# Kernel tuning notes

Hardware: AMD Instinct MI355X
Metric: run time of the kernel (lower is better)

## Reference

```python
import jax, jax.numpy as jnp
import numpy as np

BN_EPS = 1e-5


def setup_inputs() -> dict:
    key = jax.random.key(0)
    ks = jax.random.split(key, 7)
    B, C, N = 8, 512, 2048
    P = C // 2
    x = jax.random.normal(ks[0], (B, C, N), dtype=jnp.float32)
    # 1x1 conv weights (no bias), shape [out, in]
    Wg = jax.random.normal(ks[1], (P, C), dtype=jnp.float32) * (1.0 / np.sqrt(C))
    Wtheta = jax.random.normal(ks[2], (P, C), dtype=jnp.float32) * (1.0 / np.sqrt(C))
    Wphi = jax.random.normal(ks[3], (P, C), dtype=jnp.float32) * (1.0 / np.sqrt(C))
    Wz = jax.random.normal(ks[4], (C, P), dtype=jnp.float32) * (1.0 / np.sqrt(P))
    gamma = jnp.ones((C,), dtype=jnp.float32)
    beta = jnp.zeros((C,), dtype=jnp.float32)
    return {"x": x, "Wg": Wg, "Wtheta": Wtheta, "Wphi": Wphi, "Wz": Wz,
            "gamma": gamma, "beta": beta}


def reference(x, Wg, Wtheta, Wphi, Wz, gamma, beta):
    # x: [B, C, N]
    g = jnp.einsum('pc,bcn->bnp', Wg, x)        # [B, N, P]
    theta = jnp.einsum('pc,bcn->bnp', Wtheta, x)  # [B, N, P]
    phi = jnp.einsum('pc,bcn->bpn', Wphi, x)      # [B, P, N]
    f = jnp.einsum('bnp,bpm->bnm', theta, phi)    # [B, N, N] unscaled scores
    f = jax.nn.softmax(f, axis=-1)
    y = jnp.einsum('bnm,bmp->bpn', f, g)          # [B, P, N]
    z = jnp.einsum('cp,bpn->bcn', Wz, y)          # [B, C, N]
    # BatchNorm1d (training-mode batch stats over batch and length dims)
    mean = jnp.mean(z, axis=(0, 2), keepdims=True)
    var = jnp.mean((z - mean) ** 2, axis=(0, 2), keepdims=True)
    z_bn = (z - mean) / jnp.sqrt(var + BN_EPS)
    z_bn = z_bn * gamma[None, :, None] + beta[None, :, None]
    return z_bn + x
```

## Files before the change

kernel.cpp:

```cpp
#include <hip/hip_runtime.h>
#include <hip/hip_bf16.h>


typedef __attribute__((ext_vector_type(8))) short short8;
typedef __attribute__((ext_vector_type(4))) float floatx4;

__device__ __forceinline__ unsigned short f2bf(float v) {
    __hip_bfloat16 h = __float2bfloat16(v);
    return *(unsigned short*)&h;
}
__device__ __forceinline__ float bf2f(unsigned short u) {
    __hip_bfloat16 h;
    *(unsigned short*)&h = u;
    return __bfloat162float(h);
}

__device__ __forceinline__ void gl16(const unsigned short* g, unsigned short* l) {
    __builtin_amdgcn_global_load_lds(
        (const __attribute__((address_space(1))) unsigned int*)g,
        (__attribute__((address_space(3))) unsigned int*)l, 16, 0, 0);
}

__global__ __launch_bounds__(256) void transpose_split(
    const float* __restrict__ X, unsigned short* __restrict__ Thi,
    unsigned short* __restrict__ Tlo, int R, int N)
{
    X   += (long)blockIdx.z * R * N;
    Thi += (long)blockIdx.z * N * R;
    Tlo += (long)blockIdx.z * N * R;
    __shared__ float s[32][133];
    const int t = threadIdx.x;
    const int n0 = blockIdx.x * 128, r0 = blockIdx.y * 32;
    const int nf = (t & 31) * 4, rf = t >> 5;
#pragma unroll
    for (int rr = 0; rr < 4; ++rr) {
        const int row = rf + rr * 8;
        const float4 v = *(const float4*)&X[(long)(r0 + row) * N + n0 + nf];
        s[row][nf]     = v.x;
        s[row][nf + 1] = v.y;
        s[row][nf + 2] = v.z;
        s[row][nf + 3] = v.w;
    }
    __syncthreads();
    const int n = t >> 1, rs = (t & 1) * 16;
    short8 h0, h1, l0, l1;
#pragma unroll
    for (int j = 0; j < 8; ++j) {
        const float v = s[rs + j][n];
        const unsigned short h = f2bf(v);
        h0[j] = (short)h;
        l0[j] = (short)f2bf(v - bf2f(h));
    }
#pragma unroll
    for (int j = 0; j < 8; ++j) {
        const float v = s[rs + 8 + j][n];
        const unsigned short h = f2bf(v);
        h1[j] = (short)h;
        l1[j] = (short)f2bf(v - bf2f(h));
    }
    const long ob = (long)(n0 + n) * R + r0 + rs;
    *(short8*)&Thi[ob]     = h0;
    *(short8*)&Thi[ob + 8] = h1;
    *(short8*)&Tlo[ob]     = l0;
    *(short8*)&Tlo[ob + 8] = l1;
}

__global__ __launch_bounds__(256) void split_w2(
    const float* __restrict__ Wth, const float* __restrict__ Wph,
    unsigned short* __restrict__ Whi, unsigned short* __restrict__ Wlo, int PC)
{
    const int i = blockIdx.x * 256 + threadIdx.x;
    if (i < 2 * PC) {
        const float v = (i < PC) ? Wth[i] : Wph[i - PC];
        const unsigned short hi = f2bf(v);
        Whi[i] = hi;
        Wlo[i] = f2bf(v - bf2f(hi));
    }
}

__global__ __launch_bounds__(256) void cast_bf16(
    const float* __restrict__ X, unsigned short* __restrict__ Y)
{
    const long i = ((long)blockIdx.x * 256 + threadIdx.x) * 4;
    const float4 v = *(const float4*)&X[i];
    ushort4 o;
    o.x = f2bf(v.x); o.y = f2bf(v.y); o.z = f2bf(v.z); o.w = f2bf(v.w);
    *(ushort4*)&Y[i] = o;
}

#define BK 32

template <bool SPLIT, int OUTMODE, int FM, int FN, bool XYSWAP>
__global__ __launch_bounds__(256) void mfma_gemm(
    const unsigned short* __restrict__ Ahi, const unsigned short* __restrict__ Alo,
    const unsigned short* __restrict__ Bhi, const unsigned short* __restrict__ Blo,
    void* __restrict__ Cout, void* __restrict__ Cout2,
    int K, int lda, int ldb, int ldc,
    long sA, long sB, long sC,
    float* __restrict__ S1, float* __restrict__ S2)
{
    constexpr int MTM = FM * 32, MTN = FN * 32;
    constexpr int SA = FM / 2, SB = FN / 2;
    constexpr int ASZ = MTM * BK, BSZ = MTN * BK;

    Ahi += (long)blockIdx.z * sA;
    Bhi += (long)blockIdx.z * sB;
    if (SPLIT) { Alo += (long)blockIdx.z * sA; Blo += (long)blockIdx.z * sB; }
    float* Cf = (float*)Cout + (long)blockIdx.z * sC;
    unsigned short* Ch = (unsigned short*)Cout + (long)blockIdx.z * sC;
    unsigned short* Cl = (unsigned short*)Cout2 + (long)blockIdx.z * sC;

    __shared__ unsigned short AsH[2 * ASZ], BsH[2 * BSZ];
    __shared__ unsigned short AsL[SPLIT ? 2 * ASZ : 8], BsL[SPLIT ? 2 * BSZ : 8];

    const int tid = threadIdx.x;
    const int wid = tid >> 6, lane = tid & 63;
    const int wm = (wid >> 1) * (FM * 16), wn = (wid & 1) * (FN * 16);
    const int l15 = lane & 15, quad = lane >> 4;
    const int m0 = (XYSWAP ? blockIdx.x : blockIdx.y) * MTM;
    const int n0 = (XYSWAP ? blockIdx.y : blockIdx.x) * MTN;

    int arow[SA], acol[SA], brow[SB], bcol[SB];
#pragma unroll
    for (int t = 0; t < SA; ++t) {
        const int gid = t * 256 + tid;
        arow[t] = gid >> 2; acol[t] = (gid & 3) * 8;
    }
#pragma unroll
    for (int t = 0; t < SB; ++t) {
        const int gid = t * 256 + tid;
        brow[t] = gid >> 2; bcol[t] = (gid & 3) * 8;
    }

    auto stage = [&](int k0, int buf) {
#pragma unroll
        for (int t = 0; t < SA; ++t) {
            const long o = (long)(m0 + arow[t]) * lda + k0 + acol[t];
            const int d = buf * ASZ + (t * 256 + tid) * 8;
            gl16(&Ahi[o], &AsH[d]);
            if (SPLIT) gl16(&Alo[o], &AsL[d]);
        }
#pragma unroll
        for (int t = 0; t < SB; ++t) {
            const long o = (long)(n0 + brow[t]) * ldb + k0 + bcol[t];
            const int d = buf * BSZ + (t * 256 + tid) * 8;
            gl16(&Bhi[o], &BsH[d]);
            if (SPLIT) gl16(&Blo[o], &BsL[d]);
        }
    };

    floatx4 acc[FM][FN];
#pragma unroll
    for (int i = 0; i < FM; ++i)
#pragma unroll
        for (int j = 0; j < FN; ++j) acc[i][j] = (floatx4){0.f, 0.f, 0.f, 0.f};

    const int iters = K / BK;
    stage(0, 0);
    __syncthreads();

    for (int it = 0; it < iters; ++it) {
        const int cur = it & 1;
        if (it + 1 < iters) stage((it + 1) * BK, cur ^ 1);

        short8 ah[FM], bh[FN], al[SPLIT ? FM : 1], bl[SPLIT ? FN : 1];
#pragma unroll
        for (int i = 0; i < FM; ++i) {
            ah[i] = *(const short8*)&AsH[cur * ASZ + (wm + i * 16 + l15) * BK + quad * 8];
            if (SPLIT) al[i] = *(const short8*)&AsL[cur * ASZ + (wm + i * 16 + l15) * BK + quad * 8];
        }
#pragma unroll
        for (int j = 0; j < FN; ++j) {
            bh[j] = *(const short8*)&BsH[cur * BSZ + (wn + j * 16 + l15) * BK + quad * 8];
            if (SPLIT) bl[j] = *(const short8*)&BsL[cur * BSZ + (wn + j * 16 + l15) * BK + quad * 8];
        }
#pragma unroll
        for (int i = 0; i < FM; ++i)
#pragma unroll
            for (int j = 0; j < FN; ++j) {
                acc[i][j] = __builtin_amdgcn_mfma_f32_16x16x32_bf16(ah[i], bh[j], acc[i][j], 0, 0, 0);
                if (SPLIT) {
                    acc[i][j] = __builtin_amdgcn_mfma_f32_16x16x32_bf16(ah[i], bl[j], acc[i][j], 0, 0, 0);
                    acc[i][j] = __builtin_amdgcn_mfma_f32_16x16x32_bf16(al[i], bh[j], acc[i][j], 0, 0, 0);
                }
            }

        __syncthreads();
    }

#pragma unroll
    for (int i = 0; i < FM; ++i)
#pragma unroll
        for (int j = 0; j < FN; ++j) {
            const int m = m0 + wm + i * 16 + quad * 4;
            const int n = n0 + wn + j * 16 + l15;
#pragma unroll
            for (int r = 0; r < 4; ++r) {
                const float v = acc[i][j][r];
                const long idx = (long)(m + r) * ldc + n;
                if (OUTMODE == 0) {
                    Cf[idx] = v;
                } else if (OUTMODE == 1 || OUTMODE == 3) {
                    Ch[idx] = f2bf(v);
                } else {
                    const unsigned short hi = f2bf(v);
                    Ch[idx] = hi;
                    Cl[idx] = f2bf(v - bf2f(hi));
                }
            }
        }

    if (OUTMODE == 3) {
        const int slot = (blockIdx.z * gridDim.x + blockIdx.x) * 2 + (wn >> 6);
#pragma unroll
        for (int i = 0; i < FM; ++i)
#pragma unroll
            for (int r = 0; r < 4; ++r) {
                float s = 0.f, q = 0.f;
#pragma unroll
                for (int j = 0; j < FN; ++j) {
                    const float v = acc[i][j][r];
                    s += v; q += v * v;
                }
#pragma unroll
                for (int msk = 1; msk < 16; msk <<= 1) {
                    s += __shfl_xor(s, msk, 64);
                    q += __shfl_xor(q, msk, 64);
                }
                if (l15 == 0) {
                    const int row = m0 + wm + i * 16 + quad * 4 + r;
                    S1[(long)row * 256 + slot] = s;
                    S2[(long)row * 256 + slot] = q;
                }
            }
    }
}

#define PSTRP 136

__device__ __forceinline__ int swz64(int row, int slot) {
    return (row << 6) + (((slot ^ row) & 7) << 3);
}

__global__ __launch_bounds__(256, 2) void fused_attn(
    const unsigned short* __restrict__ thphH,
    const unsigned short* __restrict__ thphL,
    const unsigned short* __restrict__ gbf,
    float* __restrict__ yp,
    float2* __restrict__ ml)
{
    const int N = 2048, P = 256, P2 = 512;
    const int id = blockIdx.x;
    const int b  = id & 7;
    const int kh = (id >> 3) & 1;
    const int qt = id >> 4;
    const int q0 = qt * 64;

    const unsigned short* thB = thphH + (long)b * N * P2;
    const unsigned short* tlB = thphL + (long)b * N * P2;
    const unsigned short* gB  = gbf   + (long)b * P * N;
    float*  ypB = yp + (long)kh * (8L * N * P) + (long)b * N * P;
    float2* mlB = ml + (long)kh * (8L * N) + (long)b * N;

    __shared__ unsigned short FG[2 * 128 * 64];
    unsigned short* Fh = FG;
    unsigned short* Fl = FG + 128 * 64;
    unsigned short* Gs = FG;
    __shared__ unsigned short Pw[4][16 * PSTRP];
    __shared__ float Aly[64];

    const int tid = threadIdx.x;
    const int wid = tid >> 6, lane = tid & 63;
    const int l15 = lane & 15, quad = lane >> 4;

    short8 tHr[8], tLr[8];
    {
        const unsigned short* t1 = thB + (long)(q0 + wid * 16 + l15) * P2;
        const unsigned short* t2 = tlB + (long)(q0 + wid * 16 + l15) * P2;
#pragma unroll
        for (int kt = 0; kt < 8; ++kt) {
            tHr[kt] = *(const short8*)&t1[kt * 32 + quad * 8];
            tLr[kt] = *(const short8*)&t2[kt * 32 + quad * 8];
        }
    }

    float mrun[4], lrun[4];
#pragma unroll
    for (int r = 0; r < 4; ++r) { mrun[r] = -1e30f; lrun[r] = 0.f; }

    floatx4 oacc[16];
#pragma unroll
    for (int p = 0; p < 16; ++p) oacc[p] = (floatx4){0.f, 0.f, 0.f, 0.f};

    const int prow4 = tid >> 2, lslot = tid & 3;
    short8 pfH[2][2], pfL[2][2];
    short8 pg[2][4];

    for (int mt = 0; mt < 8; ++mt) {
        const int m0 = kh * 1024 + mt * 128;

        floatx4 sacc[8];
#pragma unroll
        for (int j = 0; j < 8; ++j) sacc[j] = (floatx4){0.f, 0.f, 0.f, 0.f};

#pragma unroll
        for (int s = 0; s < 2; ++s) {
            const long o = (long)(m0 + s * 64 + prow4) * P2 + P + 0 * 32 + lslot * 8;
            pfH[0][s] = *(const short8*)&thB[o];
            pfL[0][s] = *(const short8*)&tlB[o];
        }
#pragma unroll
        for (int s = 0; s < 2; ++s) {
            const int row = s * 64 + prow4;
            *(short8*)&Fh[swz64(row, lslot)] = pfH[0][s];
            *(short8*)&Fl[swz64(row, lslot)] = pfL[0][s];
        }
#pragma unroll
        for (int s = 0; s < 2; ++s) {
            const long o = (long)(m0 + s * 64 + prow4) * P2 + P + 1 * 32 + lslot * 8;
            pfH[1][s] = *(const short8*)&thB[o];
            pfL[1][s] = *(const short8*)&tlB[o];
        }
        __syncthreads();

#pragma unroll
        for (int kc = 0; kc < 8; ++kc) {
            if (kc < 6) {
#pragma unroll
                for (int s = 0; s < 2; ++s) {
                    const long o = (long)(m0 + s * 64 + prow4) * P2 + P + (kc + 2) * 32 + lslot * 8;
                    pfH[kc & 1][s] = *(const short8*)&thB[o];
                    pfL[kc & 1][s] = *(const short8*)&tlB[o];
                }
            }
            const short8 aH = tHr[kc];
            const short8 aL = tLr[kc];
            const int half = (kc & 1) * 4;
            __builtin_amdgcn_s_setprio(1);
#pragma unroll
            for (int j = 0; j < 8; ++j) {
                const int ro = swz64(j * 16 + l15, half + quad);
                const short8 bh = *(const short8*)&Fh[ro];
                const short8 bl = *(const short8*)&Fl[ro];
                sacc[j] = __builtin_amdgcn_mfma_f32_16x16x32_bf16(aH, bh, sacc[j], 0, 0, 0);
                sacc[j] = __builtin_amdgcn_mfma_f32_16x16x32_bf16(aH, bl, sacc[j], 0, 0, 0);
                sacc[j] = __builtin_amdgcn_mfma_f32_16x16x32_bf16(aL, bh, sacc[j], 0, 0, 0);
            }
            __builtin_amdgcn_s_setprio(0);
            if (kc < 7) {
                const int wh = ((kc + 1) & 1) * 4;
#pragma unroll
                for (int s = 0; s < 2; ++s) {
                    const int row = s * 64 + prow4;
                    *(short8*)&Fh[swz64(row, wh + lslot)] = pfH[(kc + 1) & 1][s];
                    *(short8*)&Fl[swz64(row, wh + lslot)] = pfL[(kc + 1) & 1][s];
                }
            }
            __syncthreads();
        }

        float alpha[4];
#pragma unroll
        for (int r = 0; r < 4; ++r) {
            float v = sacc[0][r];
#pragma unroll
            for (int j = 1; j < 8; ++j) v = fmaxf(v, sacc[j][r]);
            v = fmaxf(v, __shfl_xor(v, 1, 64));
            v = fmaxf(v, __shfl_xor(v, 2, 64));
            v = fmaxf(v, __shfl_xor(v, 4, 64));
            v = fmaxf(v, __shfl_xor(v, 8, 64));
            const float mo = mrun[r];
            const float mn = fmaxf(mo, v);
            mrun[r] = mn;
            alpha[r] = __expf(mo - mn);
        }
        float lpart[4] = {0.f, 0.f, 0.f, 0.f};
#pragma unroll
        for (int j = 0; j < 8; ++j)
#pragma unroll
            for (int r = 0; r < 4; ++r) {
                const float p = __expf(sacc[j][r] - mrun[r]);
                Pw[wid][(quad * 4 + r) * PSTRP + j * 16 + l15] = f2bf(p);
                lpart[r] += p;
            }
#pragma unroll
        for (int r = 0; r < 4; ++r) {
            float s = lpart[r];
            s += __shfl_xor(s, 1, 64);
            s += __shfl_xor(s, 2, 64);
            s += __shfl_xor(s, 4, 64);
            s += __shfl_xor(s, 8, 64);
            lrun[r] = lrun[r] * alpha[r] + s;
        }
        if (l15 == 0) {
#pragma unroll
            for (int r = 0; r < 4; ++r) Aly[wid * 16 + quad * 4 + r] = alpha[r];
        }

#pragma unroll
        for (int s = 0; s < 4; ++s)
            pg[0][s] = *(const short8*)&gB[(long)(s * 64 + prow4) * N + m0 + 0 * 32 + lslot * 8];
#pragma unroll
        for (int s = 0; s < 4; ++s)
            *(short8*)&Gs[swz64(s * 64 + prow4, lslot)] = pg[0][s];
#pragma unroll
        for (int s = 0; s < 4; ++s)
            pg[1][s] = *(const short8*)&gB[(long)(s * 64 + prow4) * N + m0 + 1 * 32 + lslot * 8];
        __syncthreads();

        float alr[4][4];
#pragma unroll
        for (int g = 0; g < 4; ++g)
#pragma unroll
            for (int r = 0; r < 4; ++r) alr[g][r] = Aly[g * 16 + quad * 4 + r];
        int noresc = 1;
#pragma unroll
        for (int g = 0; g < 4; ++g)
#pragma unroll
            for (int r = 0; r < 4; ++r) noresc &= (alr[g][r] == 1.f);
        if (!__all(noresc)) {
#pragma unroll
            for (int g = 0; g < 4; ++g)
#pragma unroll
                for (int pj = 0; pj < 4; ++pj)
#pragma unroll
                    for (int r = 0; r < 4; ++r) oacc[g * 4 + pj][r] *= alr[g][r];
        }

#pragma unroll
        for (int mc = 0; mc < 4; ++mc) {
            if (mc < 2) {
#pragma unroll
                for (int s = 0; s < 4; ++s)
                    pg[mc & 1][s] = *(const short8*)&gB[(long)(s * 64 + prow4) * N + m0 + (mc + 2) * 32 + lslot * 8];
            }
            const int half = (mc & 1) * 4;
            short8 af[4];
#pragma unroll
            for (int g = 0; g < 4; ++g)
                af[g] = *(const short8*)&Pw[g][l15 * PSTRP + mc * 32 + quad * 8];
            __builtin_amdgcn_s_setprio(1);
#pragma unroll
            for (int pj = 0; pj < 4; ++pj) {
                const short8 bg = *(const short8*)&Gs[swz64(wid * 64 + pj * 16 + l15, half + quad)];
#pragma unroll
                for (int g = 0; g < 4; ++g)
                    oacc[g * 4 + pj] = __builtin_amdgcn_mfma_f32_16x16x32_bf16(af[g], bg, oacc[g * 4 + pj], 0, 0, 0);
            }
            __builtin_amdgcn_s_setprio(0);
            if (mc < 3) {
                const int wh = ((mc + 1) & 1) * 4;
#pragma unroll
                for (int s = 0; s < 4; ++s)
                    *(short8*)&Gs[swz64(s * 64 + prow4, wh + lslot)] = pg[(mc + 1) & 1][s];
                __syncthreads();
            }
        }
    }

    if (l15 == 0) {
#pragma unroll
        for (int r = 0; r < 4; ++r) Aly[wid * 16 + quad * 4 + r] = 1.0f / lrun[r];
    }
    __syncthreads();
    float liv[4][4];
#pragma unroll
    for (int g = 0; g < 4; ++g)
#pragma unroll
        for (int r = 0; r < 4; ++r) liv[g][r] = Aly[g * 16 + quad * 4 + r];
#pragma unroll
    for (int g = 0; g < 4; ++g)
#pragma unroll
        for (int pj = 0; pj < 4; ++pj)
#pragma unroll
            for (int r = 0; r < 4; ++r) {
                const int row = q0 + g * 16 + quad * 4 + r;
                const int col = wid * 64 + pj * 16 + l15;
                ypB[(long)row * P + col] = oacc[g * 4 + pj][r] * liv[g][r];
            }
    if (l15 == 0) {
#pragma unroll
        for (int r = 0; r < 4; ++r) {
            const int row = q0 + wid * 16 + quad * 4 + r;
            mlB[row] = float2{mrun[r], lrun[r]};
        }
    }
}

__global__ __launch_bounds__(256) void attn_merge(
    const float* __restrict__ yp, const float2* __restrict__ ml,
    unsigned short* __restrict__ ybf)
{
    const long HALF = 8L * 2048 * 256;
    const long t = (long)blockIdx.x * 256 + threadIdx.x;
    const long row = t >> 5;
    const int  c0  = ((int)t & 31) * 8;
    const float2 a = ml[row];
    const float2 c = ml[8L * 2048 + row];
    const float mx = fmaxf(a.x, c.x);
    const float w1 = a.y * __expf(a.x - mx);
    const float w2 = c.y * __expf(c.x - mx);
    const float inv = 1.0f / (w1 + w2);
    const float f1 = w1 * inv, f2 = w2 * inv;
    const long base = row * 256 + c0;
    const float4 u0 = *(const float4*)&yp[base];
    const float4 u1 = *(const float4*)&yp[base + 4];
    const float4 v0 = *(const float4*)&yp[HALF + base];
    const float4 v1 = *(const float4*)&yp[HALF + base + 4];
    ushort4 o0, o1;
    o0.x = f2bf(f1 * u0.x + f2 * v0.x);
    o0.y = f2bf(f1 * u0.y + f2 * v0.y);
    o0.z = f2bf(f1 * u0.z + f2 * v0.z);
    o0.w = f2bf(f1 * u0.w + f2 * v0.w);
    o1.x = f2bf(f1 * u1.x + f2 * v1.x);
    o1.y = f2bf(f1 * u1.y + f2 * v1.y);
    o1.z = f2bf(f1 * u1.z + f2 * v1.z);
    o1.w = f2bf(f1 * u1.w + f2 * v1.w);
    *(ushort4*)&ybf[base] = o0;
    *(ushort4*)&ybf[base + 4] = o1;
}

__global__ __launch_bounds__(256) void bn_finalize(
    const float* __restrict__ p1, const float* __restrict__ p2,
    float* __restrict__ mean, float* __restrict__ rstd, float cnt)
{
    const int c = blockIdx.x, t = threadIdx.x;
    __shared__ float rs[256], rq[256];
    rs[t] = p1[(long)c * 256 + t];
    rq[t] = p2[(long)c * 256 + t];
    __syncthreads();
    for (int st = 128; st > 0; st >>= 1) {
        if (t < st) { rs[t] += rs[t + st]; rq[t] += rq[t + st]; }
        __syncthreads();
    }
    if (t == 0) {
        const float m = rs[0] / cnt;
        mean[c] = m;
        rstd[c] = rsqrtf(rq[0] / cnt - m * m + 1e-5f);
    }
}

__global__ __launch_bounds__(256) void bn_apply_bf(
    const unsigned short* __restrict__ z, const float* __restrict__ x,
    const float* __restrict__ mean, const float* __restrict__ rstd,
    const float* __restrict__ gamma, const float* __restrict__ beta,
    float* __restrict__ out)
{
    const long i = ((long)blockIdx.x * 256 + threadIdx.x) * 8;
    const int c = (int)((i >> 11) & 511);
    const float mu = mean[c], rs = rstd[c], ga = gamma[c], be = beta[c];
    const ushort4 z0 = *(const ushort4*)&z[i];
    const ushort4 z1 = *(const ushort4*)&z[i + 4];
    const float4 x0 = *(const float4*)&x[i];
    const float4 x1 = *(const float4*)&x[i + 4];
    float4 o0, o1;
    o0.x = (bf2f(z0.x) - mu) * rs * ga + be + x0.x;
    o0.y = (bf2f(z0.y) - mu) * rs * ga + be + x0.y;
    o0.z = (bf2f(z0.z) - mu) * rs * ga + be + x0.z;
    o0.w = (bf2f(z0.w) - mu) * rs * ga + be + x0.w;
    o1.x = (bf2f(z1.x) - mu) * rs * ga + be + x1.x;
    o1.y = (bf2f(z1.y) - mu) * rs * ga + be + x1.y;
    o1.z = (bf2f(z1.z) - mu) * rs * ga + be + x1.z;
    o1.w = (bf2f(z1.w) - mu) * rs * ga + be + x1.w;
    *(float4*)&out[i] = o0;
    *(float4*)&out[i + 4] = o1;
}

extern "C" void kernel_launch(void* const* d_in, const int* in_sizes, int n_in,
                              void* d_out, int out_size, void* d_ws, size_t ws_size,
                              hipStream_t stream)
{
    const int B = 8, C = 512, N = 2048, P = 256;
    const float* x      = (const float*)d_in[0];
    const float* Wg     = (const float*)d_in[1];
    const float* Wtheta = (const float*)d_in[2];
    const float* Wphi   = (const float*)d_in[3];
    const float* Wz     = (const float*)d_in[4];
    const float* gamma  = (const float*)d_in[5];
    const float* beta   = (const float*)d_in[6];
    float* out = (float*)d_out;

    float* ws = (float*)d_ws;
    const long NCle = (long)N * C;
    const long NP   = (long)N * P;
    const long R0   = (long)B * NCle;
    unsigned short* xtH   = (unsigned short*)ws;
    unsigned short* xtL   = xtH + B * NCle;
    unsigned short* zbf   = (unsigned short*)ws;
    unsigned short* thphH = (unsigned short*)(ws + R0);
    unsigned short* thphL = thphH + B * NCle;
    unsigned short* gbf   = (unsigned short*)(ws + 2 * R0);
    unsigned short* fbf   = gbf + B * NP;
    unsigned short* ybf   = fbf + (long)B * N * N;
    unsigned short* W2H   = ybf + B * NP;
    unsigned short* W2L   = W2H + 2L * P * C;
    unsigned short* WgB   = W2L + 2L * P * C;
    unsigned short* WzB   = WgB + (long)P * C;
    float*          yp    = (float*)fbf;
    float2*         ml    = (float2*)(ws + 6L * 1024 * 1024);
    float*          bnp1  = ws + R0;
    float*          bnp2  = bnp1 + (long)C * 256;
    float*          mean  = bnp2 + (long)C * 256;
    float*          rstd  = mean + C;

    const long sX = (long)C * N;
    const int  P2 = 2 * P;

    transpose_split<<<dim3(N / 128, C / 32, B), 256, 0, stream>>>(x, xtH, xtL, C, N);
    split_w2<<<(2 * P * C + 255) / 256, 256, 0, stream>>>(Wtheta, Wphi, W2H, W2L, P * C);
    cast_bf16<<<P * C / 1024, 256, 0, stream>>>(Wg, WgB);
    cast_bf16<<<P * C / 1024, 256, 0, stream>>>(Wz, WzB);

    mfma_gemm<true, 2, 4, 4, true><<<dim3(N / 128, P2 / 128, B), 256, 0, stream>>>(
        xtH, xtL, W2H, W2L, thphH, thphL, C, C, C, P2, NCle, 0, NCle, nullptr, nullptr);
    mfma_gemm<false, 1, 2, 4, false><<<dim3(N / 128, P / 64, B), 256, 0, stream>>>(
        WgB, WgB, xtH, xtH, gbf, gbf, C, C, C, N, 0, NCle, NP, nullptr, nullptr);

    fused_attn<<<dim3(512), 256, 0, stream>>>(thphH, thphL, gbf, yp, ml);
    attn_merge<<<dim3(2048), 256, 0, stream>>>(yp, ml, ybf);

    mfma_gemm<false, 3, 4, 4, false><<<dim3(N / 128, C / 128, B), 256, 0, stream>>>(
        WzB, WzB, ybf, ybf, zbf, zbf, P, P, P, N, 0, NP, sX, bnp1, bnp2);

    bn_finalize<<<C, 256, 0, stream>>>(bnp1, bnp2, mean, rstd, (float)B * N);
    bn_apply_bf<<<(int)((B * sX) / 2048), 256, 0, stream>>>(zbf, x, mean, rstd, gamma, beta, out);
}
```

Before: 265.6 us.

## Split attention keys four ways and make PV accumulation per-wave

Splits the key dimension of the fused attention kernel into four chunks instead of two, doubling the grid, and extends the merge kernel to combine four partial results. Each wave now accumulates all 256 output columns for its own 16 query rows. This removes the shared alpha and inverse-sum exchange through LDS and the extra barrier, and the P tile moves to a swizzled per-wave layout. The three weight-prep kernels are fused into one launch. In exchange, partial-output traffic to global memory doubles, the merge reads twice as much, and each wave issues more LDS reads of G per MFMA step.

```diff
diff --git a/kernel.cpp b/kernel.cpp
--- a/kernel.cpp
+++ b/kernel.cpp
@@ -65,27 +65,31 @@
     *(short8*)&Tlo[ob + 8] = l1;
 }
 
-__global__ __launch_bounds__(256) void split_w2(
+__global__ __launch_bounds__(256) void prep_weights(
     const float* __restrict__ Wth, const float* __restrict__ Wph,
-    unsigned short* __restrict__ Whi, unsigned short* __restrict__ Wlo, int PC)
+    const float* __restrict__ Wg,  const float* __restrict__ Wz,
+    unsigned short* __restrict__ Whi, unsigned short* __restrict__ Wlo,
+    unsigned short* __restrict__ WgB, unsigned short* __restrict__ WzB, int PC)
 {
     const int i = blockIdx.x * 256 + threadIdx.x;
-    if (i < 2 * PC) {
+    {
         const float v = (i < PC) ? Wth[i] : Wph[i - PC];
         const unsigned short hi = f2bf(v);
         Whi[i] = hi;
         Wlo[i] = f2bf(v - bf2f(hi));
     }
-}
-
-__global__ __launch_bounds__(256) void cast_bf16(
-    const float* __restrict__ X, unsigned short* __restrict__ Y)
-{
-    const long i = ((long)blockIdx.x * 256 + threadIdx.x) * 4;
-    const float4 v = *(const float4*)&X[i];
-    ushort4 o;
-    o.x = f2bf(v.x); o.y = f2bf(v.y); o.z = f2bf(v.z); o.w = f2bf(v.w);
-    *(ushort4*)&Y[i] = o;
+    if (i < PC / 4) {
+        const float4 v = *(const float4*)&Wg[i * 4];
+        ushort4 o;
+        o.x = f2bf(v.x); o.y = f2bf(v.y); o.z = f2bf(v.z); o.w = f2bf(v.w);
+        *(ushort4*)&WgB[i * 4] = o;
+    } else if (i < PC / 2) {
+        const int j = i - PC / 4;
+        const float4 v = *(const float4*)&Wz[j * 4];
+        ushort4 o;
+        o.x = f2bf(v.x); o.y = f2bf(v.y); o.z = f2bf(v.z); o.w = f2bf(v.w);
+        *(ushort4*)&WzB[j * 4] = o;
+    }
 }
 
 #define BK 32
@@ -236,10 +240,12 @@
     }
 }
 
-#define PSTRP 136
 
 __device__ __forceinline__ int swz64(int row, int slot) {
     return (row << 6) + (((slot ^ row) & 7) << 3);
+}
+__device__ __forceinline__ int swzP(int row, int g) {
+    return (row << 7) + (((g & 8) | ((g ^ row) & 7)) << 3);
 }
 
 __global__ __launch_bounds__(256, 2) void fused_attn(
@@ -252,8 +258,8 @@
     const int N = 2048, P = 256, P2 = 512;
     const int id = blockIdx.x;
     const int b  = id & 7;
-    const int kh = (id >> 3) & 1;
-    const int qt = id >> 4;
+    const int kh = (id >> 3) & 3;
+    const int qt = id >> 5;
     const int q0 = qt * 64;
 
     const unsigned short* thB = thphH + (long)b * N * P2;
@@ -266,12 +272,12 @@
     unsigned short* Fh = FG;
     unsigned short* Fl = FG + 128 * 64;
     unsigned short* Gs = FG;
-    __shared__ unsigned short Pw[4][16 * PSTRP];
-    __shared__ float Aly[64];
+    __shared__ unsigned short Pw[4 * 16 * 128];
 
     const int tid = threadIdx.x;
     const int wid = tid >> 6, lane = tid & 63;
     const int l15 = lane & 15, quad = lane >> 4;
+    unsigned short* Pwv = Pw + wid * 16 * 128;
 
     short8 tHr[8], tLr[8];
     {
@@ -296,8 +302,8 @@
     short8 pfH[2][2], pfL[2][2];
     short8 pg[2][4];
 
-    for (int mt = 0; mt < 8; ++mt) {
-        const int m0 = kh * 1024 + mt * 128;
+    for (int mt = 0; mt < 4; ++mt) {
+        const int m0 = kh * 512 + mt * 128;
 
         floatx4 sacc[8];
 #pragma unroll
@@ -380,7 +386,9 @@
 #pragma unroll
             for (int r = 0; r < 4; ++r) {
                 const float p = __expf(sacc[j][r] - mrun[r]);
-                Pw[wid][(quad * 4 + r) * PSTRP + j * 16 + l15] = f2bf(p);
+                const int row = quad * 4 + r;
+                const int g = j * 2 + (l15 >> 3);
+                Pwv[swzP(row, g) + (l15 & 7)] = f2bf(p);
                 lpart[r] += p;
             }
 #pragma unroll
@@ -392,9 +400,16 @@
             s += __shfl_xor(s, 8, 64);
             lrun[r] = lrun[r] * alpha[r] + s;
         }
-        if (l15 == 0) {
-#pragma unroll
-            for (int r = 0; r < 4; ++r) Aly[wid * 16 + quad * 4 + r] = alpha[r];
+
+        {
+            const int noresc = (alpha[0] == 1.f) & (alpha[1] == 1.f) &
+                               (alpha[2] == 1.f) & (alpha[3] == 1.f);
+            if (!__all(noresc)) {
+#pragma unroll
+                for (int p = 0; p < 16; ++p)
+#pragma unroll
+                    for (int r = 0; r < 4; ++r) oacc[p][r] *= alpha[r];
+            }
         }
 
 #pragma unroll
@@ -408,25 +423,6 @@
             pg[1][s] = *(const short8*)&gB[(long)(s * 64 + prow4) * N + m0 + 1 * 32 + lslot * 8];
         __syncthreads();
 
-        float alr[4][4];
-#pragma unroll
-        for (int g = 0; g < 4; ++g)
-#pragma unroll
-            for (int r = 0; r < 4; ++r) alr[g][r] = Aly[g * 16 + quad * 4 + r];
-        int noresc = 1;
-#pragma unroll
-        for (int g = 0; g < 4; ++g)
-#pragma unroll
-            for (int r = 0; r < 4; ++r) noresc &= (alr[g][r] == 1.f);
-        if (!__all(noresc)) {
-#pragma unroll
-            for (int g = 0; g < 4; ++g)
-#pragma unroll
-                for (int pj = 0; pj < 4; ++pj)
-#pragma unroll
-                    for (int r = 0; r < 4; ++r) oacc[g * 4 + pj][r] *= alr[g][r];
-        }
-
 #pragma unroll
         for (int mc = 0; mc < 4; ++mc) {
             if (mc < 2) {
@@ -435,17 +431,12 @@
                     pg[mc & 1][s] = *(const short8*)&gB[(long)(s * 64 + prow4) * N + m0 + (mc + 2) * 32 + lslot * 8];
             }
             const int half = (mc & 1) * 4;
-            short8 af[4];
-#pragma unroll
-            for (int g = 0; g < 4; ++g)
-                af[g] = *(const short8*)&Pw[g][l15 * PSTRP + mc * 32 + quad * 8];
+            const short8 af = *(const short8*)&Pwv[swzP(l15, mc * 4 + quad)];
             __builtin_amdgcn_s_setprio(1);
 #pragma unroll
-            for (int pj = 0; pj < 4; ++pj) {
-                const short8 bg = *(const short8*)&Gs[swz64(wid * 64 + pj * 16 + l15, half + quad)];
-#pragma unroll
-                for (int g = 0; g < 4; ++g)
-                    oacc[g * 4 + pj] = __builtin_amdgcn_mfma_f32_16x16x32_bf16(af[g], bg, oacc[g * 4 + pj], 0, 0, 0);
+            for (int pj = 0; pj < 16; ++pj) {
+                const short8 bg = *(const short8*)&Gs[swz64(pj * 16 + l15, half + quad)];
+                oacc[pj] = __builtin_amdgcn_mfma_f32_16x16x32_bf16(af, bg, oacc[pj], 0, 0, 0);
             }
             __builtin_amdgcn_s_setprio(0);
             if (mc < 3) {
@@ -458,26 +449,17 @@
         }
     }
 
-    if (l15 == 0) {
-#pragma unroll
-        for (int r = 0; r < 4; ++r) Aly[wid * 16 + quad * 4 + r] = 1.0f / lrun[r];
-    }
-    __syncthreads();
-    float liv[4][4];
-#pragma unroll
-    for (int g = 0; g < 4; ++g)
-#pragma unroll
-        for (int r = 0; r < 4; ++r) liv[g][r] = Aly[g * 16 + quad * 4 + r];
-#pragma unroll
-    for (int g = 0; g < 4; ++g)
-#pragma unroll
-        for (int pj = 0; pj < 4; ++pj)
-#pragma unroll
-            for (int r = 0; r < 4; ++r) {
-                const int row = q0 + g * 16 + quad * 4 + r;
-                const int col = wid * 64 + pj * 16 + l15;
-                ypB[(long)row * P + col] = oacc[g * 4 + pj][r] * liv[g][r];
-            }
+    float linv[4];
+#pragma unroll
+    for (int r = 0; r < 4; ++r) linv[r] = 1.0f / lrun[r];
+#pragma unroll
+    for (int pj = 0; pj < 16; ++pj)
+#pragma unroll
+        for (int r = 0; r < 4; ++r) {
+            const int row = q0 + wid * 16 + quad * 4 + r;
+            const int col = pj * 16 + l15;
+            ypB[(long)row * P + col] = oacc[pj][r] * linv[r];
+        }
     if (l15 == 0) {
 #pragma unroll
         for (int r = 0; r < 4; ++r) {
@@ -491,31 +473,40 @@
     const float* __restrict__ yp, const float2* __restrict__ ml,
     unsigned short* __restrict__ ybf)
 {
-    const long HALF = 8L * 2048 * 256;
+    const long STRIDE = 8L * 2048 * 256;
+    const long NROWS  = 8L * 2048;
     const long t = (long)blockIdx.x * 256 + threadIdx.x;
     const long row = t >> 5;
     const int  c0  = ((int)t & 31) * 8;
-    const float2 a = ml[row];
-    const float2 c = ml[8L * 2048 + row];
-    const float mx = fmaxf(a.x, c.x);
-    const float w1 = a.y * __expf(a.x - mx);
-    const float w2 = c.y * __expf(c.x - mx);
-    const float inv = 1.0f / (w1 + w2);
-    const float f1 = w1 * inv, f2 = w2 * inv;
+    const float2 a0 = ml[row];
+    const float2 a1 = ml[NROWS + row];
+    const float2 a2 = ml[2 * NROWS + row];
+    const float2 a3 = ml[3 * NROWS + row];
+    const float mx = fmaxf(fmaxf(a0.x, a1.x), fmaxf(a2.x, a3.x));
+    const float w0 = a0.y * __expf(a0.x - mx);
+    const float w1 = a1.y * __expf(a1.x - mx);
+    const float w2 = a2.y * __expf(a2.x - mx);
+    const float w3 = a3.y * __expf(a3.x - mx);
+    const float inv = 1.0f / (w0 + w1 + w2 + w3);
+    const float f0 = w0 * inv, f1 = w1 * inv, f2 = w2 * inv, f3 = w3 * inv;
     const long base = row * 256 + c0;
     const float4 u0 = *(const float4*)&yp[base];
     const float4 u1 = *(const float4*)&yp[base + 4];
-    const float4 v0 = *(const float4*)&yp[HALF + base];
-    const float4 v1 = *(const float4*)&yp[HALF + base + 4];
+    const float4 v0 = *(const float4*)&yp[STRIDE + base];
+    const float4 v1 = *(const float4*)&yp[STRIDE + base + 4];
+    const float4 p0 = *(const float4*)&yp[2 * STRIDE + base];
+    const float4 p1 = *(const float4*)&yp[2 * STRIDE + base + 4];
+    const float4 q0 = *(const float4*)&yp[3 * STRIDE + base];
+    const float4 q1 = *(const float4*)&yp[3 * STRIDE + base + 4];
     ushort4 o0, o1;
-    o0.x = f2bf(f1 * u0.x + f2 * v0.x);
-    o0.y = f2bf(f1 * u0.y + f2 * v0.y);
-    o0.z = f2bf(f1 * u0.z + f2 * v0.z);
-    o0.w = f2bf(f1 * u0.w + f2 * v0.w);
-    o1.x = f2bf(f1 * u1.x + f2 * v1.x);
-    o1.y = f2bf(f1 * u1.y + f2 * v1.y);
-    o1.z = f2bf(f1 * u1.z + f2 * v1.z);
-    o1.w = f2bf(f1 * u1.w + f2 * v1.w);
+    o0.x = f2bf(f0 * u0.x + f1 * v0.x + f2 * p0.x + f3 * q0.x);
+    o0.y = f2bf(f0 * u0.y + f1 * v0.y + f2 * p0.y + f3 * q0.y);
+    o0.z = f2bf(f0 * u0.z + f1 * v0.z + f2 * p0.z + f3 * q0.z);
+    o0.w = f2bf(f0 * u0.w + f1 * v0.w + f2 * p0.w + f3 * q0.w);
+    o1.x = f2bf(f0 * u1.x + f1 * v1.x + f2 * p1.x + f3 * q1.x);
+    o1.y = f2bf(f0 * u1.y + f1 * v1.y + f2 * p1.y + f3 * q1.y);
+    o1.z = f2bf(f0 * u1.z + f1 * v1.z + f2 * p1.z + f3 * q1.z);
+    o1.w = f2bf(f0 * u1.w + f1 * v1.w + f2 * p1.w + f3 * q1.w);
     *(ushort4*)&ybf[base] = o0;
     *(ushort4*)&ybf[base + 4] = o1;
 }
@@ -607,16 +598,15 @@
     const int  P2 = 2 * P;
 
     transpose_split<<<dim3(N / 128, C / 32, B), 256, 0, stream>>>(x, xtH, xtL, C, N);
-    split_w2<<<(2 * P * C + 255) / 256, 256, 0, stream>>>(Wtheta, Wphi, W2H, W2L, P * C);
-    cast_bf16<<<P * C / 1024, 256, 0, stream>>>(Wg, WgB);
-    cast_bf16<<<P * C / 1024, 256, 0, stream>>>(Wz, WzB);
+    prep_weights<<<(2 * P * C) / 256, 256, 0, stream>>>(
+        Wtheta, Wphi, Wg, Wz, W2H, W2L, WgB, WzB, P * C);
 
     mfma_gemm<true, 2, 4, 4, true><<<dim3(N / 128, P2 / 128, B), 256, 0, stream>>>(
         xtH, xtL, W2H, W2L, thphH, thphL, C, C, C, P2, NCle, 0, NCle, nullptr, nullptr);
     mfma_gemm<false, 1, 2, 4, false><<<dim3(N / 128, P / 64, B), 256, 0, stream>>>(
         WgB, WgB, xtH, xtH, gbf, gbf, C, C, C, N, 0, NCle, NP, nullptr, nullptr);
 
-    fused_attn<<<dim3(512), 256, 0, stream>>>(thphH, thphL, gbf, yp, ml);
+    fused_attn<<<dim3(1024), 256, 0, stream>>>(thphH, thphL, gbf, yp, ml);
     attn_merge<<<dim3(2048), 256, 0, stream>>>(yp, ml, ybf);
 
     mfma_gemm<false, 3, 4, 4, false><<<dim3(N / 128, C / 128, B), 256, 0, stream>>>(
```

Result: slower. 314.9 us (+18.6%).
